# Optimization experiments

Hardware: AMD Instinct MI355X
Metric: run time of the kernel (lower is better)

Reference implementation:

```python
import jax, jax.numpy as jnp
import numpy as np

B, T, D = 4, 2048, 1024

def setup_inputs() -> dict:
    key = jax.random.key(0)
    kx, kq, kk, kv = jax.random.split(key, 4)
    scale = 1.0 / np.sqrt(D)
    return {
        "x": jax.random.normal(kx, (B, T, D), dtype=jnp.float32),
        "Wq": jax.random.normal(kq, (D, D), dtype=jnp.float32) * scale,
        "Wk": jax.random.normal(kk, (D, D), dtype=jnp.float32) * scale,
        "Wv": jax.random.normal(kv, (D, D), dtype=jnp.float32) * scale,
    }

def reference(x, Wq, Wk, Wv):
    # torch Linear: y = x @ W.T (no bias, qkv_bias=False)
    q = jnp.einsum("btd,od->bto", x, Wq)
    k = jnp.einsum("btd,od->bto", x, Wk)
    v = jnp.einsum("btd,od->bto", x, Wv)
    scores = jnp.einsum("bqd,bkd->bqk", q, k)
    # NOTE: source uses non-in-place masked_fill whose result is discarded,
    # so NO causal mask is actually applied. Faithfully reproduced here.
    inv_sqrt_d = 1.0 / np.sqrt(k.shape[-1]).astype(np.float32)
    weights = jax.nn.softmax(scores * inv_sqrt_d, axis=-1)
    # dropout p=0.0 -> identity
    return jnp.einsum("bqk,bkd->bqd", weights, v)
```

## Files before the change

### kernel.cpp

```cpp
#include <hip/hip_runtime.h>
#include <hip/hip_bf16.h>
#include <hip/hip_fp16.h>
#include <type_traits>

typedef _Float16 f16;
typedef __attribute__((ext_vector_type(8))) _Float16 f16x8;
typedef __attribute__((ext_vector_type(4))) float floatx4;

#define B_ 4
#define T_ 2048
#define D_ 1024

#define XB_OFF   0ul
#define WB_OFF   16777216ul
#define QKV_OFF  23068672ul
#define S_OFF    73400320ul
#define VT_OFF   0ul

#define ASYNC16(gp, lp) \
    __builtin_amdgcn_global_load_lds((const __attribute__((address_space(1))) unsigned int*)(gp), \
                                     (__attribute__((address_space(3))) unsigned int*)(lp), 16, 0, 0)

template<int N> __device__ __forceinline__ void vmwait() {
    if constexpr (N == 0)      asm volatile("s_waitcnt vmcnt(0)" ::: "memory");
    else if constexpr (N == 4) asm volatile("s_waitcnt vmcnt(4)" ::: "memory");
    else if constexpr (N == 6) asm volatile("s_waitcnt vmcnt(6)" ::: "memory");
    else static_assert(N == 0, "unsupported vmcnt literal");
}
#define BAR()  __builtin_amdgcn_s_barrier()

__global__ __launch_bounds__(256) void cast_all(
    const float* __restrict__ x, const float* __restrict__ wq,
    const float* __restrict__ wk, const float* __restrict__ wv,
    f16* __restrict__ xb, f16* __restrict__ wb)
{
    long i = (long)blockIdx.x * 256 + threadIdx.x;
    const float4* src; f16* dst;
    if (i < 2097152L)            { src = (const float4*)x;  dst = xb; }
    else if (i < 2359296L)       { i -= 2097152L; src = (const float4*)wq; dst = wb; }
    else if (i < 2621440L)       { i -= 2359296L; src = (const float4*)wk; dst = wb + 1048576; }
    else                         { i -= 2621440L; src = (const float4*)wv; dst = wb + 2097152; }
    float4 v = src[i];
    union { f16 h[4]; uint2 u; } o;
    o.h[0] = (f16)v.x; o.h[1] = (f16)v.y; o.h[2] = (f16)v.z; o.h[3] = (f16)v.w;
    ((uint2*)dst)[i] = o.u;
}

template <typename CT>
__global__ __launch_bounds__(512, 2) void gemm8_nt(
    const f16* __restrict__ A, int lda, long sA,
    const f16* __restrict__ B, int ldb, long sB,
    CT* __restrict__ C, int ldc, long sC,
    int K, float alpha)
{
    __shared__ f16 lds[2][32768];

    const int tid = threadIdx.x;
    const int m0 = blockIdx.y * 256;
    const int n0 = blockIdx.x * 256;
    const int bz = blockIdx.z;
    A += (long)bz * sA; B += (long)bz * sB; C += (long)bz * sC;

    const int w  = tid >> 6;
    const int l  = tid & 63;
    const int wm = w >> 2;
    const int wn = w & 3;
    const int lr = l & 15;
    const int kg = l >> 4;
    const int kx = kg ^ ((lr >> 1) & 3);

    floatx4 acc[8][4] = {};

    const int srow = tid >> 2;
    const int gsl  = (tid & 3) ^ ((tid >> 3) & 3);
    const long ldaL = lda, ldbL = ldb;
    const f16* Ag = A + (long)(m0 + srow) * ldaL + gsl * 8;
    const f16* Bg = B + (long)(n0 + srow) * ldbL + gsl * 8;

    auto stA = [&](int buf, int h, int t) {
        f16* d = &lds[buf][h * 8192 + w * 512];
        const f16* g = Ag + (long)(h * 128) * ldaL + t * 64;
        ASYNC16(g,      d);
        ASYNC16(g + 32, d + 4096);
    };
    auto stB = [&](int buf, int h, int t) {
        f16* d = &lds[buf][16384 + h * 8192 + w * 512];
        const f16* g = Bg + (long)(h * 128) * ldbL + t * 64;
        ASYNC16(g,      d);
        ASYNC16(g + 32, d + 4096);
    };

    const int NT = K >> 6;
    stA(0, 0, 0); stA(0, 1, 0); stB(0, 0, 0); stB(0, 1, 0);
    stB(1, 0, 1); stB(1, 1, 1);
    vmwait<4>();
    BAR();

    const int abase = wm * 8192;
    const int bbase = 16384 + (wn >> 1) * 8192 + (wn & 1) * 2048;
    f16x8 af[2][4], bf0[2][2], bf1[2][2];

    for (int u = 0; u < NT; ++u) {
        const int cur = u & 1;
        const f16* Lc = lds[cur];

        #pragma unroll
        for (int kk = 0; kk < 2; kk++) {
            #pragma unroll
            for (int mi = 0; mi < 4; mi++)
                af[kk][mi] = *(const f16x8*)&Lc[abase + kk * 4096 + (mi * 16 + lr) * 32 + kx * 8];
            #pragma unroll
            for (int ni = 0; ni < 2; ni++)
                bf0[kk][ni] = *(const f16x8*)&Lc[bbase + kk * 4096 + (ni * 16 + lr) * 32 + kx * 8];
        }
        if (u + 1 < NT) stA(cur ^ 1, 0, u + 1);
        BAR();
        __builtin_amdgcn_s_setprio(1);
        #pragma unroll
        for (int kk = 0; kk < 2; kk++)
            #pragma unroll
            for (int mi = 0; mi < 4; mi++)
                #pragma unroll
                for (int ni = 0; ni < 2; ni++)
                    acc[mi][ni] = __builtin_amdgcn_mfma_f32_16x16x32_f16(af[kk][mi], bf0[kk][ni], acc[mi][ni], 0, 0, 0);
        __builtin_amdgcn_s_setprio(0);
        BAR();

        #pragma unroll
        for (int kk = 0; kk < 2; kk++)
            #pragma unroll
            for (int ni = 0; ni < 2; ni++)
                bf1[kk][ni] = *(const f16x8*)&Lc[bbase + kk * 4096 + ((ni + 2) * 16 + lr) * 32 + kx * 8];
        if (u + 1 < NT) stA(cur ^ 1, 1, u + 1);
        BAR();
        __builtin_amdgcn_s_setprio(1);
        #pragma unroll
        for (int kk = 0; kk < 2; kk++)
            #pragma unroll
            for (int mi = 0; mi < 4; mi++)
                #pragma unroll
                for (int ni = 0; ni < 2; ni++)
                    acc[mi][ni + 2] = __builtin_amdgcn_mfma_f32_16x16x32_f16(af[kk][mi], bf1[kk][ni], acc[mi][ni + 2], 0, 0, 0);
        __builtin_amdgcn_s_setprio(0);
        BAR();

        #pragma unroll
        for (int kk = 0; kk < 2; kk++)
            #pragma unroll
            for (int mi = 0; mi < 4; mi++)
                af[kk][mi] = *(const f16x8*)&Lc[abase + kk * 4096 + ((mi + 4) * 16 + lr) * 32 + kx * 8];
        if (u + 2 < NT) stB(cur, 0, u + 2);
        BAR();
        __builtin_amdgcn_s_setprio(1);
        #pragma unroll
        for (int kk = 0; kk < 2; kk++)
            #pragma unroll
            for (int mi = 0; mi < 4; mi++)
                #pragma unroll
                for (int ni = 0; ni < 2; ni++)
                    acc[mi + 4][ni + 2] = __builtin_amdgcn_mfma_f32_16x16x32_f16(af[kk][mi], bf1[kk][ni], acc[mi + 4][ni + 2], 0, 0, 0);
        __builtin_amdgcn_s_setprio(0);
        BAR();

        if (u + 2 < NT) stB(cur, 1, u + 2);
        BAR();
        __builtin_amdgcn_s_setprio(1);
        #pragma unroll
        for (int kk = 0; kk < 2; kk++)
            #pragma unroll
            for (int mi = 0; mi < 4; mi++)
                #pragma unroll
                for (int ni = 0; ni < 2; ni++)
                    acc[mi + 4][ni] = __builtin_amdgcn_mfma_f32_16x16x32_f16(af[kk][mi], bf0[kk][ni], acc[mi + 4][ni], 0, 0, 0);
        __builtin_amdgcn_s_setprio(0);
        if (u + 2 < NT)      vmwait<4>();
        else if (u + 1 < NT) vmwait<0>();
        BAR();
    }

    #pragma unroll
    for (int mi = 0; mi < 8; mi++)
        #pragma unroll
        for (int ni = 0; ni < 4; ni++)
            #pragma unroll
            for (int r = 0; r < 4; r++) {
                int row = m0 + wm * 128 + mi * 16 + kg * 4 + r;
                int col = n0 + wn * 64 + ni * 16 + lr;
                float v = acc[mi][ni][r] * alpha;
                if constexpr (std::is_same<CT, float>::value)
                    C[(long)row * ldc + col] = v;
                else
                    C[(long)row * ldc + col] = (f16)v;
            }
}

template <typename CT, int BN, int WN>
__global__ __launch_bounds__(256, 3) void gemm_nt(
    const f16* __restrict__ A, int lda, long sA,
    const f16* __restrict__ B, int ldb, long sB,
    CT* __restrict__ C, int ldc, long sC,
    int K, float alpha)
{
    __shared__ f16 As[3][128 * 32];
    __shared__ f16 Bs[3][BN * 32];
    constexpr int L = 2 + BN / 64;

    const int tid = threadIdx.x;
    const int m0 = blockIdx.y * 128;
    const int n0 = blockIdx.x * BN;
    const int bz = blockIdx.z;
    A += (long)bz * sA;
    B += (long)bz * sB;
    C += (long)bz * sC;

    const int w  = tid >> 6;
    const int l  = tid & 63;
    const int wm = (w >> 1) * 64;
    const int wn = (w & 1) * WN;
    const int lr = l & 15;
    const int kg = l >> 4;
    const int kx = kg ^ ((lr >> 1) & 3);

    constexpr int NI = WN / 16;
    floatx4 acc[4][NI] = {};

    const int srow = tid >> 2;
    const int gsl  = (tid & 3) ^ ((tid >> 3) & 3);
    const long ldaL = lda, ldbL = ldb;
    const f16* Aptr = A + (long)(m0 + srow) * ldaL + gsl * 8;
    const f16* Bptr = B + (long)(n0 + srow) * ldbL + gsl * 8;

    auto stage = [&](f16* Ad, f16* Bd, int kk) {
        #pragma unroll
        for (int rh = 0; rh < 2; rh++)
            ASYNC16(Aptr + kk + rh * 64 * ldaL, Ad + rh * 2048 + w * 512);
        #pragma unroll
        for (int rh = 0; rh < BN / 64; rh++)
            ASYNC16(Bptr + kk + rh * 64 * ldbL, Bd + rh * 2048 + w * 512);
    };

    f16 *a0 = As[0], *a1 = As[1], *a2 = As[2];
    f16 *b0 = Bs[0], *b1 = Bs[1], *b2 = Bs[2];

    const int NT = K >> 5;
    stage(a0, b0, 0);
    stage(a1, b1, 32);

    for (int t = 0; t < NT; ++t) {
        if (t < NT - 1) vmwait<L>(); else vmwait<0>();
        __builtin_amdgcn_s_barrier();

        if (t + 2 < NT) stage(a2, b2, (t + 2) << 5);

        f16x8 af[4], bf[NI];
        #pragma unroll
        for (int mi = 0; mi < 4; mi++)
            af[mi] = *(const f16x8*)&a0[(wm + mi * 16 + lr) * 32 + kx * 8];
        #pragma unroll
        for (int ni = 0; ni < NI; ni++)
            bf[ni] = *(const f16x8*)&b0[(wn + ni * 16 + lr) * 32 + kx * 8];
        #pragma unroll
        for (int mi = 0; mi < 4; mi++)
            #pragma unroll
            for (int ni = 0; ni < NI; ni++)
                acc[mi][ni] = __builtin_amdgcn_mfma_f32_16x16x32_f16(af[mi], bf[ni], acc[mi][ni], 0, 0, 0);

        f16* ta = a0; a0 = a1; a1 = a2; a2 = ta;
        f16* tb = b0; b0 = b1; b1 = b2; b2 = tb;
    }

    #pragma unroll
    for (int mi = 0; mi < 4; mi++) {
        #pragma unroll
        for (int ni = 0; ni < NI; ni++) {
            #pragma unroll
            for (int r = 0; r < 4; r++) {
                int row = m0 + wm + mi * 16 + kg * 4 + r;
                int col = n0 + wn + ni * 16 + lr;
                float v = acc[mi][ni][r] * alpha;
                if constexpr (std::is_same<CT, float>::value)
                    C[(long)row * ldc + col] = v;
                else
                    C[(long)row * ldc + col] = (f16)v;
            }
        }
    }
}

__global__ __launch_bounds__(256) void transpose_v(const f16* __restrict__ qkv, f16* __restrict__ vt)
{
    __shared__ f16 tile[32][33];
    int b  = blockIdx.z;
    int j0 = blockIdx.x * 32;
    int d0 = blockIdx.y * 32;
    int tx = threadIdx.x & 31;
    int ty = threadIdx.x >> 5;
    #pragma unroll
    for (int i = 0; i < 4; i++) {
        int j = j0 + ty + i * 8;
        tile[ty + i * 8][tx] = qkv[((long)b * T_ + j) * 3072 + 2048 + d0 + tx];
    }
    __syncthreads();
    #pragma unroll
    for (int i = 0; i < 4; i++) {
        int d = d0 + ty + i * 8;
        vt[((long)b * D_ + d) * T_ + j0 + tx] = tile[tx][ty + i * 8];
    }
}

__global__ __launch_bounds__(256) void softmax_rows(f16* __restrict__ S)
{
    long row = (long)blockIdx.x * 4 + (threadIdx.x >> 6);
    int l = threadIdx.x & 63;
    uint4* p4 = (uint4*)(S + row * 2048);
    union U { uint4 u; f16 h[8]; } d[4];
    float v[32];
    float mx = -1e30f;
    #pragma unroll
    for (int i = 0; i < 4; i++) {
        d[i].u = p4[i * 64 + l];
        #pragma unroll
        for (int j = 0; j < 8; j++) { v[i * 8 + j] = (float)d[i].h[j]; mx = fmaxf(mx, v[i * 8 + j]); }
    }
    #pragma unroll
    for (int off = 32; off; off >>= 1) mx = fmaxf(mx, __shfl_xor(mx, off, 64));
    float s = 0.f;
    #pragma unroll
    for (int i = 0; i < 32; i++) { v[i] = __expf(v[i] - mx); s += v[i]; }
    #pragma unroll
    for (int off = 32; off; off >>= 1) s += __shfl_xor(s, off, 64);
    float inv = 1.f / s;
    #pragma unroll
    for (int i = 0; i < 4; i++) {
        #pragma unroll
        for (int j = 0; j < 8; j++) d[i].h[j] = (f16)(v[i * 8 + j] * inv);
        p4[i * 64 + l] = d[i].u;
    }
}

extern "C" void kernel_launch(void* const* d_in, const int* in_sizes, int n_in,
                              void* d_out, int out_size, void* d_ws, size_t ws_size,
                              hipStream_t stream)
{
    const float* x  = (const float*)d_in[0];
    const float* wq = (const float*)d_in[1];
    const float* wk = (const float*)d_in[2];
    const float* wv = (const float*)d_in[3];
    float* out = (float*)d_out;
    char* ws = (char*)d_ws;
    f16* xb  = (f16*)(ws + XB_OFF);
    f16* wb  = (f16*)(ws + WB_OFF);
    f16* qkv = (f16*)(ws + QKV_OFF);
    f16* s   = (f16*)(ws + S_OFF);
    f16* vt  = (f16*)(ws + VT_OFF);

    cast_all<<<11264, 256, 0, stream>>>(x, wq, wk, wv, xb, wb);

    gemm8_nt<f16><<<dim3(12, 32, 1), 512, 0, stream>>>(
        xb, 1024, 0L, wb, 1024, 0L, qkv, 3072, 0L, 1024, 1.0f);

    transpose_v<<<dim3(64, 32, 4), 256, 0, stream>>>(qkv, vt);

    gemm8_nt<f16><<<dim3(8, 8, 4), 512, 0, stream>>>(
        qkv,        3072, (long)T_ * 3072,
        qkv + 1024, 3072, (long)T_ * 3072,
        s,          2048, (long)T_ * 2048, 1024, 0.03125f);

    softmax_rows<<<2048, 256, 0, stream>>>(s);

    gemm_nt<float, 128, 64><<<dim3(8, 16, 4), 256, 0, stream>>>(
        s,  2048, (long)T_ * 2048,
        vt, 2048, (long)D_ * 2048,
        out, 1024, (long)T_ * 1024, 2048, 1.0f);
}
```

Measured before the change: 267.0 us.

## Replace PV GEMM with 8-wave 128x256 ping-pong kernel using staged prefetch

Swaps the final softmax-by-V GEMM from a 256-thread 128x128 triple-buffered kernel to a 512-thread 128x256 kernel. The K loop is split into four quadrant phases that interleave LDS fragment reads, async global-to-LDS prefetch and MFMA bursts raised with s_setprio. The aim is better overlap of memory and matrix work and fewer, larger tiles. In exchange it adds many barriers per iteration and halves the grid, which may reduce occupancy and CU utilization. The TAG template parameter on gemm8_nt only creates separate instantiations.

```diff
diff --git a/kernel.cpp b/kernel.cpp
--- a/kernel.cpp
+++ b/kernel.cpp
@@ -46,7 +46,7 @@
     ((uint2*)dst)[i] = o.u;
 }
 
-template <typename CT>
+template <typename CT, int TAG>
 __global__ __launch_bounds__(512, 2) void gemm8_nt(
     const f16* __restrict__ A, int lda, long sA,
     const f16* __restrict__ B, int ldb, long sB,
@@ -194,97 +194,149 @@
             }
 }
 
-template <typename CT, int BN, int WN>
-__global__ __launch_bounds__(256, 3) void gemm_nt(
+template <typename CT>
+__global__ __launch_bounds__(512, 2) void gemm8b_nt(
     const f16* __restrict__ A, int lda, long sA,
     const f16* __restrict__ B, int ldb, long sB,
     CT* __restrict__ C, int ldc, long sC,
     int K, float alpha)
 {
-    __shared__ f16 As[3][128 * 32];
-    __shared__ f16 Bs[3][BN * 32];
-    constexpr int L = 2 + BN / 64;
+    __shared__ f16 lds[2][24576];
 
     const int tid = threadIdx.x;
     const int m0 = blockIdx.y * 128;
-    const int n0 = blockIdx.x * BN;
+    const int n0 = blockIdx.x * 256;
     const int bz = blockIdx.z;
-    A += (long)bz * sA;
-    B += (long)bz * sB;
-    C += (long)bz * sC;
+    A += (long)bz * sA; B += (long)bz * sB; C += (long)bz * sC;
 
     const int w  = tid >> 6;
     const int l  = tid & 63;
-    const int wm = (w >> 1) * 64;
-    const int wn = (w & 1) * WN;
+    const int wm = w >> 2;
+    const int wn = w & 3;
     const int lr = l & 15;
     const int kg = l >> 4;
     const int kx = kg ^ ((lr >> 1) & 3);
 
-    constexpr int NI = WN / 16;
-    floatx4 acc[4][NI] = {};
+    floatx4 acc[4][4] = {};
 
     const int srow = tid >> 2;
     const int gsl  = (tid & 3) ^ ((tid >> 3) & 3);
     const long ldaL = lda, ldbL = ldb;
-    const f16* Aptr = A + (long)(m0 + srow) * ldaL + gsl * 8;
-    const f16* Bptr = B + (long)(n0 + srow) * ldbL + gsl * 8;
-
-    auto stage = [&](f16* Ad, f16* Bd, int kk) {
-        #pragma unroll
-        for (int rh = 0; rh < 2; rh++)
-            ASYNC16(Aptr + kk + rh * 64 * ldaL, Ad + rh * 2048 + w * 512);
-        #pragma unroll
-        for (int rh = 0; rh < BN / 64; rh++)
-            ASYNC16(Bptr + kk + rh * 64 * ldbL, Bd + rh * 2048 + w * 512);
+    const f16* Ag = A + (long)(m0 + srow) * ldaL + gsl * 8;
+    const f16* Bg = B + (long)(n0 + srow) * ldbL + gsl * 8;
+
+    auto stA = [&](int buf, int kk, int t) {
+        ASYNC16(Ag + kk * 32 + t * 64, &lds[buf][kk * 4096 + w * 512]);
     };
-
-    f16 *a0 = As[0], *a1 = As[1], *a2 = As[2];
-    f16 *b0 = Bs[0], *b1 = Bs[1], *b2 = Bs[2];
-
-    const int NT = K >> 5;
-    stage(a0, b0, 0);
-    stage(a1, b1, 32);
-
-    for (int t = 0; t < NT; ++t) {
-        if (t < NT - 1) vmwait<L>(); else vmwait<0>();
-        __builtin_amdgcn_s_barrier();
-
-        if (t + 2 < NT) stage(a2, b2, (t + 2) << 5);
-
-        f16x8 af[4], bf[NI];
-        #pragma unroll
-        for (int mi = 0; mi < 4; mi++)
-            af[mi] = *(const f16x8*)&a0[(wm + mi * 16 + lr) * 32 + kx * 8];
-        #pragma unroll
-        for (int ni = 0; ni < NI; ni++)
-            bf[ni] = *(const f16x8*)&b0[(wn + ni * 16 + lr) * 32 + kx * 8];
-        #pragma unroll
-        for (int mi = 0; mi < 4; mi++)
-            #pragma unroll
-            for (int ni = 0; ni < NI; ni++)
-                acc[mi][ni] = __builtin_amdgcn_mfma_f32_16x16x32_f16(af[mi], bf[ni], acc[mi][ni], 0, 0, 0);
-
-        f16* ta = a0; a0 = a1; a1 = a2; a2 = ta;
-        f16* tb = b0; b0 = b1; b1 = b2; b2 = tb;
-    }
-
-    #pragma unroll
-    for (int mi = 0; mi < 4; mi++) {
-        #pragma unroll
-        for (int ni = 0; ni < NI; ni++) {
+    auto stB = [&](int buf, int kk, int t) {
+        const f16* g = Bg + kk * 32 + t * 64;
+        f16* d = &lds[buf][8192 + kk * 8192 + w * 512];
+        ASYNC16(g,                   d);
+        ASYNC16(g + 128 * ldbL,      d + 4096);
+    };
+
+    const int NT = K >> 6;
+    stA(0, 0, 0); stA(0, 1, 0); stB(0, 0, 0); stB(0, 1, 0);
+    stB(1, 0, 1); stB(1, 1, 1);
+    vmwait<4>();
+    BAR();
+
+    const int arow = wm * 64;
+    const int brow = wn * 64;
+    f16x8 af0[2][2], af1[2][2], bf0[2][2], bf1[2][2];
+
+    for (int u = 0; u < NT; ++u) {
+        const int cur = u & 1;
+        const f16* Lc = lds[cur];
+
+        #pragma unroll
+        for (int kk = 0; kk < 2; kk++) {
+            #pragma unroll
+            for (int mi = 0; mi < 2; mi++)
+                af0[kk][mi] = *(const f16x8*)&Lc[kk * 4096 + (arow + mi * 16 + lr) * 32 + kx * 8];
+            #pragma unroll
+            for (int ni = 0; ni < 2; ni++)
+                bf0[kk][ni] = *(const f16x8*)&Lc[8192 + kk * 8192 + (brow + ni * 16 + lr) * 32 + kx * 8];
+        }
+        if (u + 1 < NT) stA(cur ^ 1, 0, u + 1);
+        BAR();
+        __builtin_amdgcn_s_setprio(1);
+        #pragma unroll
+        for (int kk = 0; kk < 2; kk++)
+            #pragma unroll
+            for (int mi = 0; mi < 2; mi++)
+                #pragma unroll
+                for (int ni = 0; ni < 2; ni++)
+                    acc[mi][ni] = __builtin_amdgcn_mfma_f32_16x16x32_f16(af0[kk][mi], bf0[kk][ni], acc[mi][ni], 0, 0, 0);
+        __builtin_amdgcn_s_setprio(0);
+        BAR();
+
+        #pragma unroll
+        for (int kk = 0; kk < 2; kk++)
+            #pragma unroll
+            for (int ni = 0; ni < 2; ni++)
+                bf1[kk][ni] = *(const f16x8*)&Lc[8192 + kk * 8192 + (brow + (ni + 2) * 16 + lr) * 32 + kx * 8];
+        if (u + 1 < NT) stA(cur ^ 1, 1, u + 1);
+        BAR();
+        __builtin_amdgcn_s_setprio(1);
+        #pragma unroll
+        for (int kk = 0; kk < 2; kk++)
+            #pragma unroll
+            for (int mi = 0; mi < 2; mi++)
+                #pragma unroll
+                for (int ni = 0; ni < 2; ni++)
+                    acc[mi][ni + 2] = __builtin_amdgcn_mfma_f32_16x16x32_f16(af0[kk][mi], bf1[kk][ni], acc[mi][ni + 2], 0, 0, 0);
+        __builtin_amdgcn_s_setprio(0);
+        BAR();
+
+        #pragma unroll
+        for (int kk = 0; kk < 2; kk++)
+            #pragma unroll
+            for (int mi = 0; mi < 2; mi++)
+                af1[kk][mi] = *(const f16x8*)&Lc[kk * 4096 + (arow + (mi + 2) * 16 + lr) * 32 + kx * 8];
+        if (u + 2 < NT) stB(cur, 0, u + 2);
+        BAR();
+        __builtin_amdgcn_s_setprio(1);
+        #pragma unroll
+        for (int kk = 0; kk < 2; kk++)
+            #pragma unroll
+            for (int mi = 0; mi < 2; mi++)
+                #pragma unroll
+                for (int ni = 0; ni < 2; ni++)
+                    acc[mi + 2][ni + 2] = __builtin_amdgcn_mfma_f32_16x16x32_f16(af1[kk][mi], bf1[kk][ni], acc[mi + 2][ni + 2], 0, 0, 0);
+        __builtin_amdgcn_s_setprio(0);
+        BAR();
+
+        if (u + 2 < NT) stB(cur, 1, u + 2);
+        BAR();
+        __builtin_amdgcn_s_setprio(1);
+        #pragma unroll
+        for (int kk = 0; kk < 2; kk++)
+            #pragma unroll
+            for (int mi = 0; mi < 2; mi++)
+                #pragma unroll
+                for (int ni = 0; ni < 2; ni++)
+                    acc[mi + 2][ni] = __builtin_amdgcn_mfma_f32_16x16x32_f16(af1[kk][mi], bf0[kk][ni], acc[mi + 2][ni], 0, 0, 0);
+        __builtin_amdgcn_s_setprio(0);
+        if (u + 2 < NT)      vmwait<4>();
+        else if (u + 1 < NT) vmwait<0>();
+        BAR();
+    }
+
+    #pragma unroll
+    for (int mi = 0; mi < 4; mi++)
+        #pragma unroll
+        for (int ni = 0; ni < 4; ni++)
             #pragma unroll
             for (int r = 0; r < 4; r++) {
-                int row = m0 + wm + mi * 16 + kg * 4 + r;
-                int col = n0 + wn + ni * 16 + lr;
+                int row = m0 + wm * 64 + mi * 16 + kg * 4 + r;
+                int col = n0 + wn * 64 + ni * 16 + lr;
                 float v = acc[mi][ni][r] * alpha;
                 if constexpr (std::is_same<CT, float>::value)
                     C[(long)row * ldc + col] = v;
                 else
                     C[(long)row * ldc + col] = (f16)v;
             }
-        }
-    }
 }
 
 __global__ __launch_bounds__(256) void transpose_v(const f16* __restrict__ qkv, f16* __restrict__ vt)
@@ -356,19 +408,19 @@
 
     cast_all<<<11264, 256, 0, stream>>>(x, wq, wk, wv, xb, wb);
 
-    gemm8_nt<f16><<<dim3(12, 32, 1), 512, 0, stream>>>(
+    gemm8_nt<f16, 0><<<dim3(12, 32, 1), 512, 0, stream>>>(
         xb, 1024, 0L, wb, 1024, 0L, qkv, 3072, 0L, 1024, 1.0f);
 
     transpose_v<<<dim3(64, 32, 4), 256, 0, stream>>>(qkv, vt);
 
-    gemm8_nt<f16><<<dim3(8, 8, 4), 512, 0, stream>>>(
+    gemm8_nt<f16, 1><<<dim3(8, 8, 4), 512, 0, stream>>>(
         qkv,        3072, (long)T_ * 3072,
         qkv + 1024, 3072, (long)T_ * 3072,
         s,          2048, (long)T_ * 2048, 1024, 0.03125f);
 
     softmax_rows<<<2048, 256, 0, stream>>>(s);
 
-    gemm_nt<float, 128, 64><<<dim3(8, 16, 4), 256, 0, stream>>>(
+    gemm8b_nt<float><<<dim3(4, 16, 4), 512, 0, stream>>>(
         s,  2048, (long)T_ * 2048,
         vt, 2048, (long)D_ * 2048,
         out, 1024, (long)T_ * 1024, 2048, 1.0f);
```

After: 260.6 us. -2.4%, faster.
